# Kernel optimization log

Hardware: AMD Instinct MI355X
Metric: run time of the kernel (lower is better)

The kernel has to match this reference:

```python
import jax, jax.numpy as jnp
import numpy as np

DIM = 1024
HEADS = 16
HEAD_DIM = DIM // HEADS


def setup_inputs() -> dict:
    key = jax.random.key(0)
    ks = jax.random.split(key, 5)
    B, N = 4, 2048
    x = jax.random.normal(ks[0], (B, N, DIM), dtype=jnp.float32)
    # nn.Linear default init scale ~ 1/sqrt(fan_in)
    s = 1.0 / np.sqrt(DIM)
    W_qkv = jax.random.uniform(ks[1], (DIM, 3 * DIM), minval=-s, maxval=s, dtype=jnp.float32)
    b_qkv = jax.random.uniform(ks[2], (3 * DIM,), minval=-s, maxval=s, dtype=jnp.float32)
    W_proj = jax.random.uniform(ks[3], (DIM, DIM), minval=-s, maxval=s, dtype=jnp.float32)
    b_proj = jax.random.uniform(ks[4], (DIM,), minval=-s, maxval=s, dtype=jnp.float32)
    return {"x": x, "W_qkv": W_qkv, "b_qkv": b_qkv, "W_proj": W_proj, "b_proj": b_proj}


def reference(x, W_qkv, b_qkv, W_proj, b_proj):
    B, N, C = x.shape
    qkv = x @ W_qkv + b_qkv                      # [B, N, 3C]
    qkv = qkv.reshape(B, N, 3, HEADS, HEAD_DIM)
    q = jnp.transpose(qkv[:, :, 0], (0, 2, 1, 3))  # [B, H, N, D]
    k = jnp.transpose(qkv[:, :, 1], (0, 2, 1, 3))
    v = jnp.transpose(qkv[:, :, 2], (0, 2, 1, 3))
    scale = 1.0 / np.sqrt(HEAD_DIM)
    scores = jnp.einsum('bhqd,bhkd->bhqk', q, k) * scale  # [B, H, N, N]
    attn = jax.nn.softmax(scores, axis=-1)
    out = jnp.einsum('bhqk,bhkd->bhqd', attn, v)           # [B, H, N, D]
    out = jnp.transpose(out, (0, 2, 1, 3)).reshape(B, N, C)
    return out @ W_proj + b_proj
```

## Files before the change

kernel.cpp:

```cpp
#include <hip/hip_runtime.h>

typedef __attribute__((ext_vector_type(2)))  float  f32x2;
typedef __attribute__((ext_vector_type(4)))  float  f32x4;
typedef __attribute__((ext_vector_type(16))) float  f32x16;
typedef __attribute__((ext_vector_type(8)))  short  short8;
typedef __attribute__((ext_vector_type(4)))  unsigned int u32x4;
typedef __attribute__((ext_vector_type(2)))  unsigned int uint2v;

#define MFMA16 __builtin_amdgcn_mfma_f32_16x16x32_bf16
#define MFMA32 __builtin_amdgcn_mfma_f32_32x32x16_bf16

static __device__ __forceinline__ unsigned short f2bf(float f){
  union { float f; unsigned u; } v; v.f = f;
  unsigned r = v.u + 0x7fffu + ((v.u >> 16) & 1u);
  return (unsigned short)(r >> 16);
}

static __device__ __forceinline__ unsigned cvtpk(float a, float b){
  unsigned r;
  asm("v_cvt_pk_bf16_f32 %0, %1, %2" : "=v"(r) : "v"(a), "v"(b));
  return r;
}

static __device__ __forceinline__ void plswap(unsigned &a, unsigned &b){
  asm("v_permlane32_swap_b32 %0, %1" : "+v"(a), "+v"(b));
}

typedef __attribute__((address_space(1))) void gvoid_t;
typedef __attribute__((address_space(3))) void lvoid_t;

static __device__ __forceinline__ void gll16(const unsigned short* g, unsigned short* l){
  __builtin_amdgcn_global_load_lds((gvoid_t*)g, (lvoid_t*)l, 16, 0, 0);
}


__global__ __launch_bounds__(256) void k_convert(const float* __restrict__ x,
                                                 unsigned short* __restrict__ xb){
  __shared__ __align__(16) unsigned short sm[16384];
  const int mblk = blockIdx.x >> 4, kt = blockIdx.x & 15;
  const int t = threadIdx.x;
  const int l16 = t & 15, rg = t >> 4;
  #pragma unroll
  for (int p = 0; p < 16; p++){
    int row = p * 16 + rg;
    f32x4 v = *(const f32x4*)&x[(size_t)(mblk*256 + row) * 1024 + kt*64 + l16*4];
    uint2v u; u[0] = cvtpk(v[0], v[1]); u[1] = cvtpk(v[2], v[3]);
    int g = l16 >> 1;
    *(uint2v*)&sm[row*64 + ((g ^ (row & 7)) << 3) + (l16 & 1)*4] = u;
  }
  __syncthreads();
  size_t obase = (size_t)((mblk*16 + kt)*2) * 8192;
  #pragma unroll
  for (int i = 0; i < 8; i++){
    int o = i * 256 + t;
    int kh = o >> 10, rem = o & 1023;
    int band = rem >> 6, cc = (rem >> 4) & 3, ri = rem & 15;
    int r = band*16 + ri, g = kh*4 + cc;
    short8 vv = *(const short8*)&sm[r*64 + ((g ^ (r & 7)) << 3)];
    *(short8*)&xb[obase + (size_t)kh*8192 + rem*8] = vv;
  }
}

__global__ __launch_bounds__(256) void k_transpose(const float* __restrict__ W,
                                                   unsigned short* __restrict__ Wt,
                                                   int K, int N){
  __shared__ float tile[32][33];
  int n0 = blockIdx.x * 32, k0 = blockIdx.y * 32;
  int tx = threadIdx.x, ty = threadIdx.y;
  #pragma unroll
  for (int r = 0; r < 4; r++)
    tile[ty + 8*r][tx] = W[(size_t)(k0 + ty + 8*r) * N + n0 + tx];
  __syncthreads();
  #pragma unroll
  for (int r = 0; r < 4; r++){
    int nn = ty + 8*r;
    int n = n0 + nn, k = k0 + tx;
    int kt = k >> 6, kh = (k >> 5) & 1, cc = (k >> 3) & 3, ke = k & 7;
    int nblk = n >> 8, band = (n & 255) >> 4, ri = n & 15;
    Wt[(size_t)(((nblk*16 + kt)*2 + kh)) * 8192 + band*512 + cc*128 + ri*8 + ke] =
        f2bf(tile[tx][nn]);
  }
}

#define VMW(N) { __builtin_amdgcn_sched_barrier(0);                        \
                 asm volatile("s_waitcnt vmcnt(" #N ")" ::: "memory");     \
                 __builtin_amdgcn_s_barrier();                             \
                 __builtin_amdgcn_sched_barrier(0); }

template<int MODE>
__global__ __launch_bounds__(512, 2) void k_gemm(const unsigned short* __restrict__ A,
                                                 const unsigned short* __restrict__ Bt,
                                                 const float* __restrict__ bias,
                                                 void* __restrict__ outp,
                                                 int NT){
  __shared__ __align__(16) unsigned short lds[49152];
  const int t = threadIdx.x, w = t >> 6, l = t & 63;
  const int wr = w >> 2, wc = w & 3;
  const int bx = blockIdx.x, by = blockIdx.y;
  const int mblk = bx >> 1, mhalf = bx & 1;

  const unsigned short* Ab = A + (size_t)mblk*262144 + mhalf*4096 + t*8;
  const unsigned short* Bb = Bt + (size_t)by*262144 + t*8;

  f32x4 acc[4][4];
  #pragma unroll
  for (int i = 0; i < 4; i++)
    #pragma unroll
    for (int j = 0; j < 4; j++)
      acc[i][j] = (f32x4){0.f, 0.f, 0.f, 0.f};

  auto stage = [&](int sl){
    const int b = sl & 3;
    const size_t off = (size_t)sl * 8192;
    gll16(Ab + off,        &lds[b*12288 + t*8]);
    gll16(Bb + off,        &lds[b*12288 + 4096 + t*8]);
    gll16(Bb + off + 4096, &lds[b*12288 + 8192 + t*8]);
  };

  auto phase = [&](int b, bool do_stage, int sl){
    short8 af[4], bfr[4];
    const int aoff = b*12288 + wr*2048 + l*8;
    const int boff = b*12288 + 4096 + wc*2048 + l*8;
    #pragma unroll
    for (int i = 0; i < 4; i++) af[i]  = *(const short8*)&lds[aoff + i*512];
    #pragma unroll
    for (int j = 0; j < 4; j++) bfr[j] = *(const short8*)&lds[boff + j*512];
    if (do_stage) stage(sl);
    __builtin_amdgcn_sched_barrier(0);
    __builtin_amdgcn_s_barrier();
    __builtin_amdgcn_s_setprio(1);
    #pragma unroll
    for (int i = 0; i < 4; i++)
      #pragma unroll
      for (int j = 0; j < 4; j++)
        acc[i][j] = MFMA16(af[i], bfr[j], acc[i][j], 0, 0, 0);
    __builtin_amdgcn_s_setprio(0);
  };

  stage(0); stage(1); stage(2);
  VMW(6);

  const int NP = 2 * NT;
  int p = 0;
  for (; p <= NP - 4; ++p){
    phase(p & 3, true, p + 3);
    VMW(6);
  }
  phase(p & 3, false, 0); VMW(3); ++p;
  phase(p & 3, false, 0); VMW(0); ++p;
  phase(p & 3, false, 0);

  if (MODE == 0){
    unsigned short* qg = (unsigned short*)outp;
    unsigned short* kg = qg + (size_t)8388608;
    unsigned short* vg = kg + (size_t)8388608;
    const int which = by >> 2;
    const int lrow = l & 15;
    #pragma unroll
    for (int j = 0; j < 4; j++){
      int col = by*256 + wc*64 + j*16 + lrow;
      float bi = bias[col];
      int cc = col & 1023;
      int h = cc >> 6;
      int d = j*16 + lrow;
      if (which == 2){
        int db = d >> 5, dd = d & 31;
        #pragma unroll
        for (int i = 0; i < 4; i++){
          int nn = bx*128 + wr*64 + i*16 + (l >> 4)*4;
          int b = nn >> 11, key = nn & 2047;
          size_t idx = (size_t)(key >> 6)*4096 + (size_t)(((key >> 4) & 3)*2 + db)*512
                     + (((key >> 3) & 1)*32 + dd)*8 + (key & 7);
          uint2v u;
          u[0] = cvtpk(acc[i][j][0] + bi, acc[i][j][1] + bi);
          u[1] = cvtpk(acc[i][j][2] + bi, acc[i][j][3] + bi);
          *(uint2v*)&vg[(size_t)(b*16 + h)*131072 + idx] = u;
        }
      } else {
        unsigned short* dst = which ? kg : qg;
        float scale = which ? 1.0f : 0.18033688011f;
        int dsub = (d >> 4)*512 + ((d >> 3) & 1)*256 + (d & 7);
        #pragma unroll
        for (int i = 0; i < 4; i++)
          #pragma unroll
          for (int reg = 0; reg < 4; reg++){
            int nn = bx*128 + wr*64 + i*16 + (l >> 4)*4 + reg;
            int b = nn >> 11, row = nn & 2047;
            dst[(size_t)(b*16 + h)*131072 + (size_t)(row >> 5)*2048 + dsub + (row & 31)*8] =
                f2bf((acc[i][j][reg] + bi) * scale);
          }
      }
    }
  } else {
    float* out = (float*)outp;
    #pragma unroll
    for (int i = 0; i < 4; i++)
      #pragma unroll
      for (int reg = 0; reg < 4; reg++){
        int row = bx*128 + wr*64 + i*16 + (l >> 4)*4 + reg;
        #pragma unroll
        for (int j = 0; j < 4; j++){
          int col = by*256 + wc*64 + j*16 + (l & 15);
          out[(size_t)row * 1024 + col] = acc[i][j][reg] + bias[col];
        }
      }
  }
}

__global__ __launch_bounds__(256, 2) void k_attn(const unsigned short* __restrict__ Qg,
                                                 const unsigned short* __restrict__ Kg,
                                                 const unsigned short* __restrict__ Vg,
                                                 unsigned short* __restrict__ aout){
  __shared__ __align__(16) unsigned short lds[16384];

  const int t = threadIdx.x, w = t >> 6, l = t & 63;
  const int hi = l >> 5, q31 = l & 31;
  const int d0 = blockIdx.x;
  const int xcd = d0 & 7, jj = d0 >> 3;
  const int bh = xcd + 8*(jj >> 3);
  const int bx = jj & 7;

  const unsigned short* Qp = Qg + (size_t)bh*131072 + (size_t)bx*16384;
  const unsigned short* Kp = Kg + (size_t)bh*131072;
  const unsigned short* Vp = Vg + (size_t)bh*131072;

  #pragma unroll
  for (int i = 0; i < 8; i++){ int c = i*256 + t; gll16(Qp + c*8, &lds[c*8]); }
  __syncthreads();
  short8 qf0[4], qf1[4];
  #pragma unroll
  for (int ds = 0; ds < 4; ds++){
    qf0[ds] = *(const short8*)&lds[(2*w + 0)*2048 + ds*512 + l*8];
    qf1[ds] = *(const short8*)&lds[(2*w + 1)*2048 + ds*512 + l*8];
  }
  __syncthreads();

  #pragma unroll
  for (int i = 0; i < 2; i++){
    int c = i*256 + t;
    gll16(Kp + c*8, &lds[c*8]);
    gll16(Vp + c*8, &lds[4096 + c*8]);
  }
  __syncthreads();

  f32x16 o0lo, o0hi, o1lo, o1hi;
  #pragma unroll
  for (int i = 0; i < 16; i++){ o0lo[i]=0.f; o0hi[i]=0.f; o1lo[i]=0.f; o1hi[i]=0.f; }
  float lsum0 = 0.f, lsum1 = 0.f;

  for (int kt = 0; kt < 32; kt++){
    const int cb = (kt & 1) * 8192;
    if (kt < 31){
      const int nb = cb ^ 8192;
      #pragma unroll
      for (int i = 0; i < 2; i++){
        int c = i*256 + t;
        gll16(Kp + (size_t)(kt + 1)*4096 + c*8, &lds[nb + c*8]);
        gll16(Vp + (size_t)(kt + 1)*4096 + c*8, &lds[nb + 4096 + c*8]);
      }
    }

    f32x16 sA0, sB0, sA1, sB1;
    #pragma unroll
    for (int i = 0; i < 16; i++){ sA0[i]=0.f; sB0[i]=0.f; sA1[i]=0.f; sB1[i]=0.f; }
    __builtin_amdgcn_s_setprio(1);
    #pragma unroll
    for (int ds = 0; ds < 4; ds++){
      short8 kfA = *(const short8*)&lds[cb + ds*512 + l*8];
      short8 kfB = *(const short8*)&lds[cb + 2048 + ds*512 + l*8];
      sA0 = MFMA32(kfA, qf0[ds], sA0, 0, 0, 0);
      sB0 = MFMA32(kfB, qf0[ds], sB0, 0, 0, 0);
      sA1 = MFMA32(kfA, qf1[ds], sA1, 0, 0, 0);
      sB1 = MFMA32(kfB, qf1[ds], sB1, 0, 0, 0);
    }
    __builtin_amdgcn_s_setprio(0);

    #pragma unroll
    for (int i = 0; i < 16; i++){
      sA0[i] = __builtin_amdgcn_exp2f(sA0[i]);
      sB0[i] = __builtin_amdgcn_exp2f(sB0[i]);
      sA1[i] = __builtin_amdgcn_exp2f(sA1[i]);
      sB1[i] = __builtin_amdgcn_exp2f(sB1[i]);
    }
    {
      float r0 = (((sA0[0]+sA0[1])+(sA0[2]+sA0[3])) + ((sA0[4]+sA0[5])+(sA0[6]+sA0[7])))
               + (((sA0[8]+sA0[9])+(sA0[10]+sA0[11])) + ((sA0[12]+sA0[13])+(sA0[14]+sA0[15])))
               + (((sB0[0]+sB0[1])+(sB0[2]+sB0[3])) + ((sB0[4]+sB0[5])+(sB0[6]+sB0[7])))
               + (((sB0[8]+sB0[9])+(sB0[10]+sB0[11])) + ((sB0[12]+sB0[13])+(sB0[14]+sB0[15])));
      r0 += __shfl_xor(r0, 32);
      lsum0 += r0;
      float r1 = (((sA1[0]+sA1[1])+(sA1[2]+sA1[3])) + ((sA1[4]+sA1[5])+(sA1[6]+sA1[7])))
               + (((sA1[8]+sA1[9])+(sA1[10]+sA1[11])) + ((sA1[12]+sA1[13])+(sA1[14]+sA1[15])))
               + (((sB1[0]+sB1[1])+(sB1[2]+sB1[3])) + ((sB1[4]+sB1[5])+(sB1[6]+sB1[7])))
               + (((sB1[8]+sB1[9])+(sB1[10]+sB1[11])) + ((sB1[12]+sB1[13])+(sB1[14]+sB1[15])));
      r1 += __shfl_xor(r1, 32);
      lsum1 += r1;
    }

    u32x4 pf0[4], pf1[4];
    {
      unsigned wA[8], wB[8];
      #pragma unroll
      for (int j = 0; j < 8; j++){ wA[j] = cvtpk(sA0[2*j], sA0[2*j+1]); wB[j] = cvtpk(sB0[2*j], sB0[2*j+1]); }
      { unsigned a=wA[0],b=wA[2]; plswap(a,b); pf0[0][0]=a; pf0[0][2]=b; }
      { unsigned a=wA[1],b=wA[3]; plswap(a,b); pf0[0][1]=a; pf0[0][3]=b; }
      { unsigned a=wA[4],b=wA[6]; plswap(a,b); pf0[1][0]=a; pf0[1][2]=b; }
      { unsigned a=wA[5],b=wA[7]; plswap(a,b); pf0[1][1]=a; pf0[1][3]=b; }
      { unsigned a=wB[0],b=wB[2]; plswap(a,b); pf0[2][0]=a; pf0[2][2]=b; }
      { unsigned a=wB[1],b=wB[3]; plswap(a,b); pf0[2][1]=a; pf0[2][3]=b; }
      { unsigned a=wB[4],b=wB[6]; plswap(a,b); pf0[3][0]=a; pf0[3][2]=b; }
      { unsigned a=wB[5],b=wB[7]; plswap(a,b); pf0[3][1]=a; pf0[3][3]=b; }
    }
    {
      unsigned wA[8], wB[8];
      #pragma unroll
      for (int j = 0; j < 8; j++){ wA[j] = cvtpk(sA1[2*j], sA1[2*j+1]); wB[j] = cvtpk(sB1[2*j], sB1[2*j+1]); }
      { unsigned a=wA[0],b=wA[2]; plswap(a,b); pf1[0][0]=a; pf1[0][2]=b; }
      { unsigned a=wA[1],b=wA[3]; plswap(a,b); pf1[0][1]=a; pf1[0][3]=b; }
      { unsigned a=wA[4],b=wA[6]; plswap(a,b); pf1[1][0]=a; pf1[1][2]=b; }
      { unsigned a=wA[5],b=wA[7]; plswap(a,b); pf1[1][1]=a; pf1[1][3]=b; }
      { unsigned a=wB[0],b=wB[2]; plswap(a,b); pf1[2][0]=a; pf1[2][2]=b; }
      { unsigned a=wB[1],b=wB[3]; plswap(a,b); pf1[2][1]=a; pf1[2][3]=b; }
      { unsigned a=wB[4],b=wB[6]; plswap(a,b); pf1[3][0]=a; pf1[3][2]=b; }
      { unsigned a=wB[5],b=wB[7]; plswap(a,b); pf1[3][1]=a; pf1[3][3]=b; }
    }

    __builtin_amdgcn_s_setprio(1);
    #pragma unroll
    for (int ks = 0; ks < 4; ks++){
      short8 p0r, p1r;
      *(u32x4*)&p0r = pf0[ks];
      *(u32x4*)&p1r = pf1[ks];
      short8 vf0 = *(const short8*)&lds[cb + 4096 + (ks*2 + 0)*512 + l*8];
      short8 vf1 = *(const short8*)&lds[cb + 4096 + (ks*2 + 1)*512 + l*8];
      o0lo = MFMA32(vf0, p0r, o0lo, 0, 0, 0);
      o0hi = MFMA32(vf1, p0r, o0hi, 0, 0, 0);
      o1lo = MFMA32(vf0, p1r, o1lo, 0, 0, 0);
      o1hi = MFMA32(vf1, p1r, o1hi, 0, 0, 0);
    }
    __builtin_amdgcn_s_setprio(0);

    __syncthreads();
  }

  {
    float inv0 = 1.0f / lsum0, inv1 = 1.0f / lsum1;
    int qr0 = w*64 + q31, qr1 = w*64 + 32 + q31;
    #pragma unroll
    for (int j = 0; j < 8; j++){
      int dd0 = 8*(j >> 1) + 2*(j & 1) + 4*hi;
      int dd1 = dd0 + 32;
      *(unsigned*)&lds[qr0*64 + (((dd0 >> 3) ^ (qr0 & 7)) << 3) + (dd0 & 7)] =
          cvtpk(o0lo[2*j] * inv0, o0lo[2*j+1] * inv0);
      *(unsigned*)&lds[qr0*64 + (((dd1 >> 3) ^ (qr0 & 7)) << 3) + (dd1 & 7)] =
          cvtpk(o0hi[2*j] * inv0, o0hi[2*j+1] * inv0);
      *(unsigned*)&lds[qr1*64 + (((dd0 >> 3) ^ (qr1 & 7)) << 3) + (dd0 & 7)] =
          cvtpk(o1lo[2*j] * inv1, o1lo[2*j+1] * inv1);
      *(unsigned*)&lds[qr1*64 + (((dd1 >> 3) ^ (qr1 & 7)) << 3) + (dd1 & 7)] =
          cvtpk(o1hi[2*j] * inv1, o1hi[2*j+1] * inv1);
    }
  }
  __syncthreads();
  {
    int mblk = (bh >> 4)*8 + bx;
    int h = bh & 15;
    #pragma unroll
    for (int i = 0; i < 8; i++){
      int idx = i*256 + t;
      int kh = idx >> 10, rem = idx & 1023;
      int band = rem >> 6, cc = (rem >> 4) & 3, ri = rem & 15;
      int r = band*16 + ri, g = kh*4 + cc;
      short8 vv = *(const short8*)&lds[r*64 + ((g ^ (r & 7)) << 3)];
      size_t chunk = (size_t)((mblk*16 + h)*2 + kh);
      *(short8*)&aout[chunk*8192 + (size_t)band*512 + cc*128 + ri*8] = vv;
    }
  }
}

extern "C" void kernel_launch(void* const* d_in, const int* in_sizes, int n_in,
                              void* d_out, int out_size, void* d_ws, size_t ws_size,
                              hipStream_t stream){
  const float* x     = (const float*)d_in[0];
  const float* Wqkv  = (const float*)d_in[1];
  const float* bqkv  = (const float*)d_in[2];
  const float* Wproj = (const float*)d_in[3];
  const float* bproj = (const float*)d_in[4];

  unsigned short* ws   = (unsigned short*)d_ws;
  unsigned short* xb   = ws;
  unsigned short* Wqt  = ws + (size_t)8192 * 1024;
  unsigned short* Wpt  = Wqt + (size_t)3072 * 1024;
  unsigned short* qkvb = Wpt + (size_t)1024 * 1024;

  k_convert<<<512, 256, 0, stream>>>(x, xb);
  k_transpose<<<dim3(96, 32), dim3(32, 8), 0, stream>>>(Wqkv, Wqt, 1024, 3072);
  k_transpose<<<dim3(32, 32), dim3(32, 8), 0, stream>>>(Wproj, Wpt, 1024, 1024);
  k_gemm<0><<<dim3(64, 12), 512, 0, stream>>>(xb, Wqt, bqkv, qkvb, 16);
  k_attn<<<512, 256, 0, stream>>>(qkvb, qkvb + (size_t)8388608,
                                  qkvb + (size_t)16777216, xb);
  k_gemm<1><<<dim3(64, 4), 512, 0, stream>>>(xb, Wpt, bproj, (void*)d_out, 16);
}
```

Before: 168.3 us.

## Software-pipeline attention loop: overlap PV of previous tile with softmax of current

Restructures the attention inner loop so the PV MFMAs for the previous key tile run interleaved with exp/convert work of the current tile. V gets a triple-buffered LDS ring, with a zeroed slot for the first iteration's dummy PV, plus an epilogue PV. Explicit sched_group_barrier interleaving keeps the MFMA and VALU pipes busy together. The per-row sum shuffle is hoisted out of the loop and the score accumulators are no longer zero-initialised. The cost is more LDS and registers (double P fragments), which may pressure occupancy at 2 blocks per CU.

```diff
diff --git a/kernel.cpp b/kernel.cpp
--- a/kernel.cpp
+++ b/kernel.cpp
@@ -211,7 +211,7 @@
                                                  const unsigned short* __restrict__ Kg,
                                                  const unsigned short* __restrict__ Vg,
                                                  unsigned short* __restrict__ aout){
-  __shared__ __align__(16) unsigned short lds[16384];
+  __shared__ __align__(16) unsigned short lds[20480];
 
   const int t = threadIdx.x, w = t >> 6, l = t & 63;
   const int hi = l >> 5, q31 = l & 31;
@@ -226,6 +226,11 @@
 
   #pragma unroll
   for (int i = 0; i < 8; i++){ int c = i*256 + t; gll16(Qp + c*8, &lds[c*8]); }
+  {
+    short8 z8 = {0,0,0,0,0,0,0,0};
+    *(short8*)&lds[16384 + t*16]     = z8;
+    *(short8*)&lds[16384 + t*16 + 8] = z8;
+  }
   __syncthreads();
   short8 qf0[4], qf1[4];
   #pragma unroll
@@ -239,41 +244,60 @@
   for (int i = 0; i < 2; i++){
     int c = i*256 + t;
     gll16(Kp + c*8, &lds[c*8]);
-    gll16(Vp + c*8, &lds[4096 + c*8]);
-  }
-  __syncthreads();
-
-  f32x16 o0lo, o0hi, o1lo, o1hi;
-  #pragma unroll
-  for (int i = 0; i < 16; i++){ o0lo[i]=0.f; o0hi[i]=0.f; o1lo[i]=0.f; o1hi[i]=0.f; }
+    gll16(Vp + c*8, &lds[8192 + c*8]);
+  }
+  __syncthreads();
+
+  f32x16 ZERO;
+  #pragma unroll
+  for (int i = 0; i < 16; i++) ZERO[i] = 0.f;
+  f32x16 o0lo = ZERO, o0hi = ZERO, o1lo = ZERO, o1hi = ZERO;
   float lsum0 = 0.f, lsum1 = 0.f;
-
-  for (int kt = 0; kt < 32; kt++){
-    const int cb = (kt & 1) * 8192;
+  u32x4 pA0[4], pA1[4], pB0[4], pB1[4];
+  #pragma unroll
+  for (int ks = 0; ks < 4; ks++){
+    pA0[ks][0]=0u; pA0[ks][1]=0u; pA0[ks][2]=0u; pA0[ks][3]=0u;
+    pA1[ks][0]=0u; pA1[ks][1]=0u; pA1[ks][2]=0u; pA1[ks][3]=0u;
+  }
+  int s0 = 0, s1 = 1, s2 = 2;
+
+  auto body = [&](int kt, u32x4 (&pO0)[4], u32x4 (&pO1)[4],
+                          u32x4 (&pN0)[4], u32x4 (&pN1)[4]){
+    const int cbk = (kt & 1) * 4096;
     if (kt < 31){
-      const int nb = cb ^ 8192;
+      const int nbk = cbk ^ 4096;
+      const int nv  = 8192 + s1*4096;
       #pragma unroll
       for (int i = 0; i < 2; i++){
         int c = i*256 + t;
-        gll16(Kp + (size_t)(kt + 1)*4096 + c*8, &lds[nb + c*8]);
-        gll16(Vp + (size_t)(kt + 1)*4096 + c*8, &lds[nb + 4096 + c*8]);
+        gll16(Kp + (size_t)(kt + 1)*4096 + c*8, &lds[nbk + c*8]);
+        gll16(Vp + (size_t)(kt + 1)*4096 + c*8, &lds[nv + c*8]);
       }
     }
 
     f32x16 sA0, sB0, sA1, sB1;
-    #pragma unroll
-    for (int i = 0; i < 16; i++){ sA0[i]=0.f; sB0[i]=0.f; sA1[i]=0.f; sB1[i]=0.f; }
     __builtin_amdgcn_s_setprio(1);
-    #pragma unroll
-    for (int ds = 0; ds < 4; ds++){
-      short8 kfA = *(const short8*)&lds[cb + ds*512 + l*8];
-      short8 kfB = *(const short8*)&lds[cb + 2048 + ds*512 + l*8];
+    {
+      short8 kfA = *(const short8*)&lds[cbk + l*8];
+      short8 kfB = *(const short8*)&lds[cbk + 2048 + l*8];
+      sA0 = MFMA32(kfA, qf0[0], ZERO, 0, 0, 0);
+      sB0 = MFMA32(kfB, qf0[0], ZERO, 0, 0, 0);
+      sA1 = MFMA32(kfA, qf1[0], ZERO, 0, 0, 0);
+      sB1 = MFMA32(kfB, qf1[0], ZERO, 0, 0, 0);
+    }
+    #pragma unroll
+    for (int ds = 1; ds < 4; ds++){
+      short8 kfA = *(const short8*)&lds[cbk + ds*512 + l*8];
+      short8 kfB = *(const short8*)&lds[cbk + 2048 + ds*512 + l*8];
       sA0 = MFMA32(kfA, qf0[ds], sA0, 0, 0, 0);
       sB0 = MFMA32(kfB, qf0[ds], sB0, 0, 0, 0);
       sA1 = MFMA32(kfA, qf1[ds], sA1, 0, 0, 0);
       sB1 = MFMA32(kfB, qf1[ds], sB1, 0, 0, 0);
     }
     __builtin_amdgcn_s_setprio(0);
+    __builtin_amdgcn_sched_barrier(0);
+
+    const int pvb = 8192 + s2*4096;
 
     #pragma unroll
     for (int i = 0; i < 16; i++){
@@ -282,67 +306,93 @@
       sA1[i] = __builtin_amdgcn_exp2f(sA1[i]);
       sB1[i] = __builtin_amdgcn_exp2f(sB1[i]);
     }
-    {
-      float r0 = (((sA0[0]+sA0[1])+(sA0[2]+sA0[3])) + ((sA0[4]+sA0[5])+(sA0[6]+sA0[7])))
-               + (((sA0[8]+sA0[9])+(sA0[10]+sA0[11])) + ((sA0[12]+sA0[13])+(sA0[14]+sA0[15])))
-               + (((sB0[0]+sB0[1])+(sB0[2]+sB0[3])) + ((sB0[4]+sB0[5])+(sB0[6]+sB0[7])))
-               + (((sB0[8]+sB0[9])+(sB0[10]+sB0[11])) + ((sB0[12]+sB0[13])+(sB0[14]+sB0[15])));
-      r0 += __shfl_xor(r0, 32);
-      lsum0 += r0;
-      float r1 = (((sA1[0]+sA1[1])+(sA1[2]+sA1[3])) + ((sA1[4]+sA1[5])+(sA1[6]+sA1[7])))
-               + (((sA1[8]+sA1[9])+(sA1[10]+sA1[11])) + ((sA1[12]+sA1[13])+(sA1[14]+sA1[15])))
-               + (((sB1[0]+sB1[1])+(sB1[2]+sB1[3])) + ((sB1[4]+sB1[5])+(sB1[6]+sB1[7])))
-               + (((sB1[8]+sB1[9])+(sB1[10]+sB1[11])) + ((sB1[12]+sB1[13])+(sB1[14]+sB1[15])));
-      r1 += __shfl_xor(r1, 32);
-      lsum1 += r1;
-    }
-
-    u32x4 pf0[4], pf1[4];
+    lsum0 += ((((sA0[0]+sA0[1])+(sA0[2]+sA0[3])) + ((sA0[4]+sA0[5])+(sA0[6]+sA0[7])))
+           +  (((sA0[8]+sA0[9])+(sA0[10]+sA0[11])) + ((sA0[12]+sA0[13])+(sA0[14]+sA0[15]))))
+           + ((((sB0[0]+sB0[1])+(sB0[2]+sB0[3])) + ((sB0[4]+sB0[5])+(sB0[6]+sB0[7])))
+           +  (((sB0[8]+sB0[9])+(sB0[10]+sB0[11])) + ((sB0[12]+sB0[13])+(sB0[14]+sB0[15]))));
+    lsum1 += ((((sA1[0]+sA1[1])+(sA1[2]+sA1[3])) + ((sA1[4]+sA1[5])+(sA1[6]+sA1[7])))
+           +  (((sA1[8]+sA1[9])+(sA1[10]+sA1[11])) + ((sA1[12]+sA1[13])+(sA1[14]+sA1[15]))))
+           + ((((sB1[0]+sB1[1])+(sB1[2]+sB1[3])) + ((sB1[4]+sB1[5])+(sB1[6]+sB1[7])))
+           +  (((sB1[8]+sB1[9])+(sB1[10]+sB1[11])) + ((sB1[12]+sB1[13])+(sB1[14]+sB1[15]))));
+
     {
       unsigned wA[8], wB[8];
       #pragma unroll
       for (int j = 0; j < 8; j++){ wA[j] = cvtpk(sA0[2*j], sA0[2*j+1]); wB[j] = cvtpk(sB0[2*j], sB0[2*j+1]); }
-      { unsigned a=wA[0],b=wA[2]; plswap(a,b); pf0[0][0]=a; pf0[0][2]=b; }
-      { unsigned a=wA[1],b=wA[3]; plswap(a,b); pf0[0][1]=a; pf0[0][3]=b; }
-      { unsigned a=wA[4],b=wA[6]; plswap(a,b); pf0[1][0]=a; pf0[1][2]=b; }
-      { unsigned a=wA[5],b=wA[7]; plswap(a,b); pf0[1][1]=a; pf0[1][3]=b; }
-      { unsigned a=wB[0],b=wB[2]; plswap(a,b); pf0[2][0]=a; pf0[2][2]=b; }
-      { unsigned a=wB[1],b=wB[3]; plswap(a,b); pf0[2][1]=a; pf0[2][3]=b; }
-      { unsigned a=wB[4],b=wB[6]; plswap(a,b); pf0[3][0]=a; pf0[3][2]=b; }
-      { unsigned a=wB[5],b=wB[7]; plswap(a,b); pf0[3][1]=a; pf0[3][3]=b; }
+      { unsigned a=wA[0],b=wA[2]; plswap(a,b); pN0[0][0]=a; pN0[0][2]=b; }
+      { unsigned a=wA[1],b=wA[3]; plswap(a,b); pN0[0][1]=a; pN0[0][3]=b; }
+      { unsigned a=wA[4],b=wA[6]; plswap(a,b); pN0[1][0]=a; pN0[1][2]=b; }
+      { unsigned a=wA[5],b=wA[7]; plswap(a,b); pN0[1][1]=a; pN0[1][3]=b; }
+      { unsigned a=wB[0],b=wB[2]; plswap(a,b); pN0[2][0]=a; pN0[2][2]=b; }
+      { unsigned a=wB[1],b=wB[3]; plswap(a,b); pN0[2][1]=a; pN0[2][3]=b; }
+      { unsigned a=wB[4],b=wB[6]; plswap(a,b); pN0[3][0]=a; pN0[3][2]=b; }
+      { unsigned a=wB[5],b=wB[7]; plswap(a,b); pN0[3][1]=a; pN0[3][3]=b; }
     }
     {
       unsigned wA[8], wB[8];
       #pragma unroll
       for (int j = 0; j < 8; j++){ wA[j] = cvtpk(sA1[2*j], sA1[2*j+1]); wB[j] = cvtpk(sB1[2*j], sB1[2*j+1]); }
-      { unsigned a=wA[0],b=wA[2]; plswap(a,b); pf1[0][0]=a; pf1[0][2]=b; }
-      { unsigned a=wA[1],b=wA[3]; plswap(a,b); pf1[0][1]=a; pf1[0][3]=b; }
-      { unsigned a=wA[4],b=wA[6]; plswap(a,b); pf1[1][0]=a; pf1[1][2]=b; }
-      { unsigned a=wA[5],b=wA[7]; plswap(a,b); pf1[1][1]=a; pf1[1][3]=b; }
-      { unsigned a=wB[0],b=wB[2]; plswap(a,b); pf1[2][0]=a; pf1[2][2]=b; }
-      { unsigned a=wB[1],b=wB[3]; plswap(a,b); pf1[2][1]=a; pf1[2][3]=b; }
-      { unsigned a=wB[4],b=wB[6]; plswap(a,b); pf1[3][0]=a; pf1[3][2]=b; }
-      { unsigned a=wB[5],b=wB[7]; plswap(a,b); pf1[3][1]=a; pf1[3][3]=b; }
-    }
-
-    __builtin_amdgcn_s_setprio(1);
+      { unsigned a=wA[0],b=wA[2]; plswap(a,b); pN1[0][0]=a; pN1[0][2]=b; }
+      { unsigned a=wA[1],b=wA[3]; plswap(a,b); pN1[0][1]=a; pN1[0][3]=b; }
+      { unsigned a=wA[4],b=wA[6]; plswap(a,b); pN1[1][0]=a; pN1[1][2]=b; }
+      { unsigned a=wA[5],b=wA[7]; plswap(a,b); pN1[1][1]=a; pN1[1][3]=b; }
+      { unsigned a=wB[0],b=wB[2]; plswap(a,b); pN1[2][0]=a; pN1[2][2]=b; }
+      { unsigned a=wB[1],b=wB[3]; plswap(a,b); pN1[2][1]=a; pN1[2][3]=b; }
+      { unsigned a=wB[4],b=wB[6]; plswap(a,b); pN1[3][0]=a; pN1[3][2]=b; }
+      { unsigned a=wB[5],b=wB[7]; plswap(a,b); pN1[3][1]=a; pN1[3][3]=b; }
+    }
+
     #pragma unroll
     for (int ks = 0; ks < 4; ks++){
       short8 p0r, p1r;
-      *(u32x4*)&p0r = pf0[ks];
-      *(u32x4*)&p1r = pf1[ks];
-      short8 vf0 = *(const short8*)&lds[cb + 4096 + (ks*2 + 0)*512 + l*8];
-      short8 vf1 = *(const short8*)&lds[cb + 4096 + (ks*2 + 1)*512 + l*8];
+      *(u32x4*)&p0r = pO0[ks];
+      *(u32x4*)&p1r = pO1[ks];
+      short8 vf0 = *(const short8*)&lds[pvb + (ks*2 + 0)*512 + l*8];
+      short8 vf1 = *(const short8*)&lds[pvb + (ks*2 + 1)*512 + l*8];
       o0lo = MFMA32(vf0, p0r, o0lo, 0, 0, 0);
       o0hi = MFMA32(vf1, p0r, o0hi, 0, 0, 0);
       o1lo = MFMA32(vf0, p1r, o1lo, 0, 0, 0);
       o1hi = MFMA32(vf1, p1r, o1hi, 0, 0, 0);
     }
+
+    #pragma unroll
+    for (int g4 = 0; g4 < 4; g4++){
+      __builtin_amdgcn_sched_group_barrier(0x100, 2, 0);
+      __builtin_amdgcn_sched_group_barrier(0x002, 40, 0);
+      __builtin_amdgcn_sched_group_barrier(0x008, 4, 0);
+    }
+    __builtin_amdgcn_sched_group_barrier(0x002, 64, 0);
+
+    __syncthreads();
+    int tmp = s2; s2 = s0; s0 = s1; s1 = tmp;
+  };
+
+  for (int kt2 = 0; kt2 < 32; kt2 += 2){
+    body(kt2,     pA0, pA1, pB0, pB1);
+    body(kt2 + 1, pB0, pB1, pA0, pA1);
+  }
+
+  {
+    const int pvb = 8192 + s2*4096;
+    __builtin_amdgcn_s_setprio(1);
+    #pragma unroll
+    for (int ks = 0; ks < 4; ks++){
+      short8 p0r, p1r;
+      *(u32x4*)&p0r = pA0[ks];
+      *(u32x4*)&p1r = pA1[ks];
+      short8 vf0 = *(const short8*)&lds[pvb + (ks*2 + 0)*512 + l*8];
+      short8 vf1 = *(const short8*)&lds[pvb + (ks*2 + 1)*512 + l*8];
+      o0lo = MFMA32(vf0, p0r, o0lo, 0, 0, 0);
+      o0hi = MFMA32(vf1, p0r, o0hi, 0, 0, 0);
+      o1lo = MFMA32(vf0, p1r, o1lo, 0, 0, 0);
+      o1hi = MFMA32(vf1, p1r, o1hi, 0, 0, 0);
+    }
     __builtin_amdgcn_s_setprio(0);
-
-    __syncthreads();
-  }
-
+  }
+  __syncthreads();
+
+  lsum0 += __shfl_xor(lsum0, 32);
+  lsum1 += __shfl_xor(lsum1, 32);
   {
     float inv0 = 1.0f / lsum0, inv1 = 1.0f / lsum1;
     int qr0 = w*64 + q31, qr1 = w*64 + 32 + q31;
```

New measurement: 165.4 us. About the same (-1.7%).
